# Optimization experiments

Measured on AMD Instinct MI355X. Metric: run time of the kernel, lower is better.

## Reference

```python
import jax, jax.numpy as jnp
import numpy as np

N = 50000
E = 1_600_000
IN_C = 128
HID = 64
HEADS = 2
OUT_C = 16
NEG_SLOPE = 0.2
EPS = 1e-16


def setup_inputs() -> dict:
    key = jax.random.key(0)
    ks = jax.random.split(key, 10)
    x = jax.random.normal(ks[0], (N, IN_C), dtype=jnp.float32)
    edge_index = jax.random.randint(ks[1], (2, E), 0, N, dtype=jnp.int64)
    # layer 1: in -> HEADS * HID, concat=True
    s1 = 1.0 / np.sqrt(IN_C)
    W1 = jax.random.normal(ks[2], (IN_C, HEADS * HID), dtype=jnp.float32) * s1
    att_src1 = jax.random.normal(ks[3], (HEADS, HID), dtype=jnp.float32) * (1.0 / np.sqrt(HID))
    att_dst1 = jax.random.normal(ks[4], (HEADS, HID), dtype=jnp.float32) * (1.0 / np.sqrt(HID))
    b1 = jnp.zeros((HEADS * HID,), dtype=jnp.float32)
    # layer 2: HEADS*HID -> OUT_C, heads=1
    s2 = 1.0 / np.sqrt(HEADS * HID)
    W2 = jax.random.normal(ks[5], (HEADS * HID, OUT_C), dtype=jnp.float32) * s2
    att_src2 = jax.random.normal(ks[6], (1, OUT_C), dtype=jnp.float32) * (1.0 / np.sqrt(OUT_C))
    att_dst2 = jax.random.normal(ks[7], (1, OUT_C), dtype=jnp.float32) * (1.0 / np.sqrt(OUT_C))
    b2 = jnp.zeros((OUT_C,), dtype=jnp.float32)
    return {"x": x, "W1": W1, "att_src1": att_src1, "att_dst1": att_dst1, "b1": b1,
            "W2": W2, "att_src2": att_src2, "att_dst2": att_dst2, "b2": b2,
            "edge_index": edge_index}


def gat_conv(x, edge_index, W, att_src, att_dst, bias, heads, out_ch):
    """PyG-style GATConv: per-head linear, additive attention, softmax over
    incoming edges of each destination node, scatter-add aggregation."""
    n = x.shape[0]
    src, dst = edge_index[0], edge_index[1]
    h = (x @ W).reshape(n, heads, out_ch)                # [N,H,C]
    a_src = jnp.einsum('nhc,hc->nh', h, att_src)          # [N,H]
    a_dst = jnp.einsum('nhc,hc->nh', h, att_dst)          # [N,H]
    e = a_src[src] + a_dst[dst]                           # [E,H]
    e = jnp.where(e >= 0, e, NEG_SLOPE * e)               # LeakyReLU(0.2)
    e_max = jax.ops.segment_max(e, dst, num_segments=n)   # [N,H]
    e_max = jax.lax.stop_gradient(jnp.where(jnp.isfinite(e_max), e_max, 0.0))
    e_exp = jnp.exp(e - e_max[dst])                       # [E,H]
    denom = jax.ops.segment_sum(e_exp, dst, num_segments=n)  # [N,H]
    alpha = e_exp / (denom[dst] + EPS)                    # [E,H]
    msg = h[src] * alpha[:, :, None]                      # [E,H,C] (dominant traffic)
    out = jax.ops.segment_sum(msg, dst, num_segments=n)   # [N,H,C]
    return out.reshape(n, heads * out_ch) + bias


def reference(x, W1, att_src1, att_dst1, b1, W2, att_src2, att_dst2, b2, edge_index):
    h = gat_conv(x, edge_index, W1, att_src1, att_dst1, b1, HEADS, HID)
    h = jax.nn.elu(h)
    h = gat_conv(h, edge_index, W2, att_src2, att_dst2, b2, 1, OUT_C)
    return jax.nn.softmax(h, axis=1)
```

## Files before the change

kernel.cpp:

```cpp
#include <hip/hip_runtime.h>
#include <hip/hip_fp16.h>
#include <cstdint>
#include <cstddef>

#define N_NODES 50000
#define N_EDGES 1600000
#define NEG_SLOPE 0.2f
#define GAT_EPS 1e-16f

#define NCHUNK 128
#define CE (N_EDGES / NCHUNK)
#define NBKT 196
#define GEMM_BLOCKS 782

typedef _Float16 half8v __attribute__((ext_vector_type(8)));
typedef float f32x4 __attribute__((ext_vector_type(4)));



__global__ __launch_bounds__(256) void k_prep_tiny(
    const float* __restrict__ W1, const float* __restrict__ W2,
    const float* __restrict__ b1,
    _Float16* __restrict__ w1t, float* __restrict__ w2tp, float* __restrict__ b1p) {
    int t = threadIdx.x, b = blockIdx.x;
    if (b < 8) {
        for (int i = t; i < 2048; i += 256) {
            int idx = b * 2048 + i;
            int c = idx >> 7, k = idx & 127;
            w1t[c * 136 + k] = (_Float16)W1[k * 128 + c];
        }
    } else {
        for (int i = t; i < 2112; i += 256) {
            int j = i / 132, kp = i % 132;
            if (kp < 128) {
                int real = (kp & 7) * 16 + (kp >> 3);
                w2tp[j * 132 + kp] = W2[real * 16 + j];
            } else {
                w2tp[j * 132 + kp] = 0.f;
            }
        }
        if (t < 128) {
            int real = (t & 7) * 16 + (t >> 3);
            b1p[t] = b1[real];
        }
    }
}


__global__ __launch_bounds__(256) void k_gh(
    const float* __restrict__ x, const _Float16* __restrict__ w1t,
    const float* __restrict__ att_src, const float* __restrict__ att_dst,
    _Float16* __restrict__ h1p, float* __restrict__ a_src, float* __restrict__ a_dst,
    const int* __restrict__ ei, int* __restrict__ coarse) {
    __shared__ __align__(16) char smem[34816];
    int t = threadIdx.x;
    int b = blockIdx.x;
    if (b >= GEMM_BLOCKS) {
        int* h = (int*)smem;
        int g = b - GEMM_BLOCKS;
        if (t < NBKT) h[t] = 0;
        __syncthreads();
        int e0 = g * CE;
        for (int e = e0 + t; e < e0 + CE; e += 256)
            atomicAdd(&h[ei[N_EDGES + e] >> 8], 1);
        __syncthreads();
        if (t < NBKT) coarse[t * NCHUNK + g] = h[t];
        return;
    }
    _Float16* wl = (_Float16*)smem;
    {
        const uint4* src = (const uint4*)w1t;
        uint4* dst = (uint4*)wl;
        for (int j = t; j < 2176; j += 256) dst[j] = src[j];
    }
    __syncthreads();
    int wv = t >> 6, lane = t & 63;
    int m = lane & 15, q = lane >> 4;
    int nb = b * 64 + wv * 16;
    int grow = nb + m;
    const float* xrow = x + (size_t)((grow < N_NODES) ? grow : (N_NODES - 1)) * 128;
    f32x4 acc[8];
#pragma unroll
    for (int ct = 0; ct < 8; ++ct) acc[ct] = (f32x4){0.f, 0.f, 0.f, 0.f};
#pragma unroll
    for (int kc = 0; kc < 4; ++kc) {
        float4 u0 = *(const float4*)(xrow + kc * 32 + q * 8);
        float4 u1 = *(const float4*)(xrow + kc * 32 + q * 8 + 4);
        half8v a;
        a[0] = (_Float16)u0.x; a[1] = (_Float16)u0.y;
        a[2] = (_Float16)u0.z; a[3] = (_Float16)u0.w;
        a[4] = (_Float16)u1.x; a[5] = (_Float16)u1.y;
        a[6] = (_Float16)u1.z; a[7] = (_Float16)u1.w;
#pragma unroll
        for (int ct = 0; ct < 8; ++ct) {
            half8v bf = *(const half8v*)(wl + (ct * 16 + m) * 136 + kc * 32 + q * 8);
            acc[ct] = __builtin_amdgcn_mfma_f32_16x16x32_f16(a, bf, acc[ct], 0, 0, 0);
        }
    }
    float att_s[8], att_d[8];
#pragma unroll
    for (int ct = 0; ct < 8; ++ct) {
        att_s[ct] = att_src[ct * 16 + m];
        att_d[ct] = att_dst[ct * 16 + m];
    }
#pragma unroll
    for (int r = 0; r < 4; ++r) {
        int gn = nb + q * 4 + r;
        half8v hv;
        float ps0 = 0.f, ps1 = 0.f, pd0 = 0.f, pd1 = 0.f;
#pragma unroll
        for (int ct = 0; ct < 8; ++ct) {
            float v = acc[ct][r];
            hv[ct] = (_Float16)v;
            if (ct < 4) { ps0 += v * att_s[ct]; pd0 += v * att_d[ct]; }
            else        { ps1 += v * att_s[ct]; pd1 += v * att_d[ct]; }
        }
#pragma unroll
        for (int off = 8; off >= 1; off >>= 1) {
            ps0 += __shfl_xor(ps0, off, 64);
            ps1 += __shfl_xor(ps1, off, 64);
            pd0 += __shfl_xor(pd0, off, 64);
            pd1 += __shfl_xor(pd1, off, 64);
        }
        if (gn < N_NODES) {
            *(half8v*)(h1p + (size_t)gn * 128 + m * 8) = hv;
            if (m == 0) {
                a_src[gn * 2 + 0] = ps0;
                a_src[gn * 2 + 1] = ps1;
                a_dst[gn * 2 + 0] = pd0;
                a_dst[gn * 2 + 1] = pd1;
            }
        }
    }
}


__global__ __launch_bounds__(1024) void k_cscan(const int* __restrict__ coarse,
                                                int* __restrict__ cbase,
                                                int* __restrict__ bb,
                                                int* __restrict__ row_start) {
    __shared__ int cl[NBKT * NCHUNK];
    __shared__ int btot[NBKT];
    __shared__ int bbase[NBKT];
    int t = threadIdx.x;
    for (int i = t; i < NBKT * NCHUNK; i += 1024) cl[i] = coarse[i];
    __syncthreads();
    if (t < NBKT) {
        int s = 0;
        for (int g = 0; g < NCHUNK; ++g) s += cl[t * NCHUNK + g];
        btot[t] = s;
    }
    __syncthreads();
    if (t == 0) {
        int base = 0;
        for (int b = 0; b < NBKT; ++b) { bbase[b] = base; base += btot[b]; }
    }
    __syncthreads();
    if (t < NBKT) {
        int run = bbase[t];
        bb[t] = run;
        for (int g = 0; g < NCHUNK; ++g) {
            cbase[t * NCHUNK + g] = run;
            run += cl[t * NCHUNK + g];
        }
    }
    if (t == 0) { bb[NBKT] = N_EDGES; row_start[N_NODES] = N_EDGES; }
}

__global__ __launch_bounds__(256) void k_partition(const int* __restrict__ ei,
                                                   const int* __restrict__ cbase,
                                                   int2* __restrict__ part) {
    __shared__ int loc[NBKT];
    int t = threadIdx.x, g = blockIdx.x;
    if (t < NBKT) loc[t] = cbase[t * NCHUNK + g];
    __syncthreads();
    int e0 = g * CE;
    for (int e = e0 + t; e < e0 + CE; e += 256) {
        int s = ei[e], d = ei[N_EDGES + e];
        int slot = atomicAdd(&loc[d >> 8], 1);
        part[slot] = make_int2(s, d);
    }
}

__global__ __launch_bounds__(256) void k_local(const int2* __restrict__ part,
                                               const int* __restrict__ bb,
                                               const float* __restrict__ a_src1,
                                               const float* __restrict__ a_dst1,
                                               int* __restrict__ row_start,
                                               int4* __restrict__ csr) {
    __shared__ int hist[256];
    __shared__ int fillv[256];
    __shared__ float2 adl[256];
    __shared__ int wtot[4];
    int t = threadIdx.x, b = blockIdx.x;
    int n0 = b << 8;
    int es = bb[b], ee = bb[b + 1];
    hist[t] = 0;
    if (n0 + t < N_NODES) adl[t] = ((const float2*)a_dst1)[n0 + t];
    __syncthreads();
    for (int e = es + t; e < ee; e += 256) atomicAdd(&hist[part[e].y - n0], 1);
    __syncthreads();
    int lane = t & 63, w = t >> 6;
    int v = hist[t], x = v;
#pragma unroll
    for (int off = 1; off < 64; off <<= 1) {
        int y = __shfl_up(x, off, 64);
        if (lane >= off) x += y;
    }
    if (lane == 63) wtot[w] = x;
    __syncthreads();
    int woff = 0;
    for (int i = 0; i < w; ++i) woff += wtot[i];
    int excl = woff + x - v;
    if (n0 + t < N_NODES) row_start[n0 + t] = es + excl;
    fillv[t] = excl;
    __syncthreads();
    for (int e = es + t; e < ee; e += 256) {
        int2 sd = part[e];
        int j = sd.y - n0;
        int slot = es + atomicAdd(&fillv[j], 1);
        float2 as = ((const float2*)a_src1)[sd.x];
        float2 ad = adl[j];
        float e0 = as.x + ad.x; e0 = (e0 >= 0.f) ? e0 : NEG_SLOPE * e0;
        float e1 = as.y + ad.y; e1 = (e1 >= 0.f) ? e1 : NEG_SLOPE * e1;
        csr[slot] = make_int4(sd.x, __float_as_int(expf(e0)), __float_as_int(expf(e1)), 0);
    }
}


__global__ __launch_bounds__(256) void k_agg1f(
    const int* __restrict__ row_start, const int4* __restrict__ csr,
    const _Float16* __restrict__ h1p, const float* __restrict__ b1p,
    const float* __restrict__ w2tp,
    const float* __restrict__ att_src2, const float* __restrict__ att_dst2,
    float* __restrict__ h2, float* __restrict__ as2, float* __restrict__ ad2) {
    __shared__ float w2l[16 * 132];
    __shared__ float rows[4][128];
    int t = threadIdx.x;
    for (int i = t; i < 528; i += 256) ((float4*)w2l)[i] = ((const float4*)w2tp)[i];
    __syncthreads();
    int wv = t >> 6, lane = t & 63;
    int d = blockIdx.x * 4 + wv;
    int row = row_start[d], end = row_start[d + 1];
    int half = lane >> 5;
    int L = lane & 31;
    int c0 = L * 4;
    int head = L & 1;
    float den = 0.f;
    float4 acc = make_float4(0.f, 0.f, 0.f, 0.f);
    int i = row;
    for (; i + 8 <= end; i += 8) {
#pragma unroll
        for (int p = 0; p < 4; ++p) {
            int idx = i + 2 * p + half;
            int4 e4 = csr[idx];
            int s = e4.x;
            float we = head ? __int_as_float(e4.z) : __int_as_float(e4.y);
            uint2 u = *(const uint2*)(h1p + (size_t)s * 128 + c0);
            __half2 p0 = *(__half2*)&u.x;
            __half2 p1 = *(__half2*)&u.y;
            float2 f0 = __half22float2(p0);
            float2 f1 = __half22float2(p1);
            den += we;
            acc.x += we * f0.x; acc.y += we * f0.y;
            acc.z += we * f1.x; acc.w += we * f1.y;
        }
    }
    for (; i < end; i += 2) {
        int idx = i + half;
        bool ok = idx < end;
        int idxc = ok ? idx : i;
        int4 e4 = csr[idxc];
        int s = e4.x;
        float we = head ? __int_as_float(e4.z) : __int_as_float(e4.y);
        if (!ok) we = 0.f;
        uint2 u = *(const uint2*)(h1p + (size_t)s * 128 + c0);
        __half2 p0 = *(__half2*)&u.x;
        __half2 p1 = *(__half2*)&u.y;
        float2 f0 = __half22float2(p0);
        float2 f1 = __half22float2(p1);
        den += we;
        acc.x += we * f0.x; acc.y += we * f0.y;
        acc.z += we * f1.x; acc.w += we * f1.y;
    }
    den += __shfl_xor(den, 32, 64);
    acc.x += __shfl_xor(acc.x, 32, 64);
    acc.y += __shfl_xor(acc.y, 32, 64);
    acc.z += __shfl_xor(acc.z, 32, 64);
    acc.w += __shfl_xor(acc.w, 32, 64);
    float inv = 1.f / (den + GAT_EPS);
    float4 bv = ((const float4*)b1p)[L];
    float o0 = acc.x * inv + bv.x;
    float o1 = acc.y * inv + bv.y;
    float o2 = acc.z * inv + bv.z;
    float o3 = acc.w * inv + bv.w;
    o0 = (o0 > 0.f) ? o0 : expm1f(o0);
    o1 = (o1 > 0.f) ? o1 : expm1f(o1);
    o2 = (o2 > 0.f) ? o2 : expm1f(o2);
    o3 = (o3 > 0.f) ? o3 : expm1f(o3);
    if (half == 0) *(float4*)(&rows[wv][c0]) = make_float4(o0, o1, o2, o3);
    int j = lane & 15, q = lane >> 4;
    const float* r = rows[wv];
    const float* wt = &w2l[j * 132];
    int k0 = q * 32;
    float acc2 = 0.f;
#pragma unroll
    for (int sI = 0; sI < 8; ++sI) {
        int sp = ((sI + q) & 7) * 4;
        float4 rv = *(const float4*)(r + k0 + sp);
        float4 w4 = *(const float4*)(wt + k0 + sp);
        acc2 += rv.x * w4.x + rv.y * w4.y + rv.z * w4.z + rv.w * w4.w;
    }
    acc2 += __shfl_xor(acc2, 16, 64);
    acc2 += __shfl_xor(acc2, 32, 64);
    if (lane < 16) {
        h2[(size_t)d * 16 + j] = acc2;
        float ps = acc2 * att_src2[j];
        float pd = acc2 * att_dst2[j];
#pragma unroll
        for (int off = 8; off >= 1; off >>= 1) {
            ps += __shfl_xor(ps, off, 64);
            pd += __shfl_xor(pd, off, 64);
        }
        if (lane == 0) { as2[d] = ps; ad2[d] = pd; }
    }
}


__global__ __launch_bounds__(256) void k_agg2(
    const int* __restrict__ row_start, const int4* __restrict__ csr,
    const float* __restrict__ h2, const float* __restrict__ as2,
    const float* __restrict__ ad2, const float* __restrict__ b2,
    float* __restrict__ out) {
    int t = threadIdx.x;
    int wv = t >> 6, lane = t & 63;
    int d = blockIdx.x * 4 + wv;
    int row = row_start[d], end = row_start[d + 1];
    float ad = ad2[d];
    int c = lane & 15, q = lane >> 4;
    float den = 0.f, acc = 0.f;
    for (int base = row; base < end; base += 64) {
        int idx = base + lane;
        float w = 0.f; int s = 0;
        if (idx < end) {
            s = csr[idx].x;
            float e = as2[s] + ad;
            e = (e >= 0.f) ? e : NEG_SLOPE * e;
            w = expf(e);
        }
        den += w;
        int m = end - base; if (m > 64) m = 64;
        int jj = 0;
        for (; jj + 8 <= m; jj += 8) {
            float w0 = __shfl(w, jj + q, 64);
            int   s0 = __shfl(s, jj + q, 64);
            float w1_ = __shfl(w, jj + 4 + q, 64);
            int   s1 = __shfl(s, jj + 4 + q, 64);
            float h0 = h2[(size_t)s0 * 16 + c];
            float h1_ = h2[(size_t)s1 * 16 + c];
            acc += w0 * h0 + w1_ * h1_;
        }
        for (; jj < m; jj += 4) {
            float wj = __shfl(w, jj + q, 64);
            int sj = __shfl(s, jj + q, 64);
            acc += wj * h2[(size_t)sj * 16 + c];
        }
    }
#pragma unroll
    for (int off = 32; off >= 1; off >>= 1) den += __shfl_xor(den, off, 64);
    acc += __shfl_xor(acc, 16, 64);
    acc += __shfl_xor(acc, 32, 64);
    float v = acc / (den + GAT_EPS) + b2[c];
    float mmax = v;
#pragma unroll
    for (int off = 8; off >= 1; off >>= 1) mmax = fmaxf(mmax, __shfl_xor(mmax, off, 16));
    float ex = expf(v - mmax);
    float sum = ex;
#pragma unroll
    for (int off = 8; off >= 1; off >>= 1) sum += __shfl_xor(sum, off, 16);
    if (lane < 16) out[(size_t)d * 16 + c] = ex / sum;
}


extern "C" void kernel_launch(void* const* d_in, const int* in_sizes, int n_in,
                              void* d_out, int out_size, void* d_ws, size_t ws_size,
                              hipStream_t stream) {
    const float* x        = (const float*)d_in[0];
    const float* W1       = (const float*)d_in[1];
    const float* att_src1 = (const float*)d_in[2];
    const float* att_dst1 = (const float*)d_in[3];
    const float* b1       = (const float*)d_in[4];
    const float* W2       = (const float*)d_in[5];
    const float* att_src2 = (const float*)d_in[6];
    const float* att_dst2 = (const float*)d_in[7];
    const float* b2       = (const float*)d_in[8];
    const int*   ei       = (const int*)d_in[9];

    char* p = (char*)d_ws;
    auto alloc = [&](size_t bytes) {
        char* r = p;
        p += (bytes + 255) & ~(size_t)255;
        return r;
    };
    _Float16* h1p  = (_Float16*)alloc(sizeof(_Float16) * (size_t)N_NODES * 128);
    _Float16* w1t  = (_Float16*)alloc(sizeof(_Float16) * 128 * 136);
    float* w2tp    = (float*)alloc(sizeof(float) * 16 * 132);
    float* b1p     = (float*)alloc(sizeof(float) * 128);
    float* h2      = (float*)alloc(sizeof(float) * (size_t)N_NODES * 16);
    float* a_src   = (float*)alloc(sizeof(float) * N_NODES * 2);
    float* a_dst   = (float*)alloc(sizeof(float) * N_NODES * 2);
    float* as2     = (float*)alloc(sizeof(float) * N_NODES);
    float* ad2     = (float*)alloc(sizeof(float) * N_NODES);
    int* coarse    = (int*)alloc(sizeof(int) * NBKT * NCHUNK);
    int* cbase     = (int*)alloc(sizeof(int) * NBKT * NCHUNK);
    int* bb        = (int*)alloc(sizeof(int) * (NBKT + 1));
    int* row_start = (int*)alloc(sizeof(int) * (N_NODES + 1));
    int2* part     = (int2*)alloc(sizeof(int2) * (size_t)N_EDGES);
    int4* csr      = (int4*)alloc(sizeof(int4) * (size_t)N_EDGES);

    k_prep_tiny<<<9, 256, 0, stream>>>(W1, W2, b1, w1t, w2tp, b1p);
    k_gh<<<GEMM_BLOCKS + NCHUNK, 256, 0, stream>>>(x, w1t, att_src1, att_dst1, h1p, a_src, a_dst, ei, coarse);
    k_cscan<<<1, 1024, 0, stream>>>(coarse, cbase, bb, row_start);
    k_partition<<<NCHUNK, 256, 0, stream>>>(ei, cbase, part);
    k_local<<<NBKT, 256, 0, stream>>>(part, bb, a_src, a_dst, row_start, csr);
    k_agg1f<<<N_NODES / 4, 256, 0, stream>>>(row_start, csr, h1p, b1p, w2tp, att_src2, att_dst2, h2, as2, ad2);
    k_agg2<<<N_NODES / 4, 256, 0, stream>>>(row_start, csr, h2, as2, ad2, b2, (float*)d_out);
}
```

Measured before the change: 267.2 us.

## Fold weight prep into GEMM kernel and use nontemporal CSR loads

Removes the separate prep kernel launch. Each GEMM block now transposes and converts W1 into shared memory directly from global fp32, and one extra block prepares the W2/b1 layouts. CSR edge reads in both aggregation kernels use nontemporal loads, so the streamed edge records do not evict the reused feature rows from cache. In exchange, every GEMM block repeats the W1 transpose with uncoalesced, bank-conflicting shared stores instead of a contiguous copy.

```diff
diff --git a/kernel.cpp b/kernel.cpp
--- a/kernel.cpp
+++ b/kernel.cpp
@@ -14,47 +14,38 @@
 #define GEMM_BLOCKS 782
 
 typedef _Float16 half8v __attribute__((ext_vector_type(8)));
+typedef _Float16 half4v __attribute__((ext_vector_type(4)));
 typedef float f32x4 __attribute__((ext_vector_type(4)));
-
-
-
-__global__ __launch_bounds__(256) void k_prep_tiny(
-    const float* __restrict__ W1, const float* __restrict__ W2,
-    const float* __restrict__ b1,
-    _Float16* __restrict__ w1t, float* __restrict__ w2tp, float* __restrict__ b1p) {
-    int t = threadIdx.x, b = blockIdx.x;
-    if (b < 8) {
-        for (int i = t; i < 2048; i += 256) {
-            int idx = b * 2048 + i;
-            int c = idx >> 7, k = idx & 127;
-            w1t[c * 136 + k] = (_Float16)W1[k * 128 + c];
-        }
-    } else {
+typedef int i32x4 __attribute__((ext_vector_type(4)));
+
+
+
+__global__ __launch_bounds__(256) void k_gh(
+    const float* __restrict__ x, const float* __restrict__ W1,
+    const float* __restrict__ W2, const float* __restrict__ b1,
+    const float* __restrict__ att_src, const float* __restrict__ att_dst,
+    _Float16* __restrict__ h1p, float* __restrict__ a_src, float* __restrict__ a_dst,
+    const int* __restrict__ ei, int* __restrict__ coarse,
+    float* __restrict__ w2tp, float* __restrict__ b1p) {
+    __shared__ __align__(16) char smem[34816];
+    int t = threadIdx.x;
+    int b = blockIdx.x;
+    if (b == GEMM_BLOCKS + NCHUNK) {
         for (int i = t; i < 2112; i += 256) {
             int j = i / 132, kp = i % 132;
+            float v = 0.f;
             if (kp < 128) {
                 int real = (kp & 7) * 16 + (kp >> 3);
-                w2tp[j * 132 + kp] = W2[real * 16 + j];
-            } else {
-                w2tp[j * 132 + kp] = 0.f;
+                v = W2[real * 16 + j];
             }
+            w2tp[i] = v;
         }
         if (t < 128) {
             int real = (t & 7) * 16 + (t >> 3);
             b1p[t] = b1[real];
         }
-    }
-}
-
-
-__global__ __launch_bounds__(256) void k_gh(
-    const float* __restrict__ x, const _Float16* __restrict__ w1t,
-    const float* __restrict__ att_src, const float* __restrict__ att_dst,
-    _Float16* __restrict__ h1p, float* __restrict__ a_src, float* __restrict__ a_dst,
-    const int* __restrict__ ei, int* __restrict__ coarse) {
-    __shared__ __align__(16) char smem[34816];
-    int t = threadIdx.x;
-    int b = blockIdx.x;
+        return;
+    }
     if (b >= GEMM_BLOCKS) {
         int* h = (int*)smem;
         int g = b - GEMM_BLOCKS;
@@ -68,10 +59,9 @@
         return;
     }
     _Float16* wl = (_Float16*)smem;
-    {
-        const uint4* src = (const uint4*)w1t;
-        uint4* dst = (uint4*)wl;
-        for (int j = t; j < 2176; j += 256) dst[j] = src[j];
+    for (int j = t; j < 16384; j += 256) {
+        int k = j >> 7, c = j & 127;
+        wl[c * 136 + k] = (_Float16)W1[j];
     }
     __syncthreads();
     int wv = t >> 6, lane = t & 63;
@@ -229,7 +219,7 @@
 
 
 __global__ __launch_bounds__(256) void k_agg1f(
-    const int* __restrict__ row_start, const int4* __restrict__ csr,
+    const int* __restrict__ row_start, const int* __restrict__ csr_i,
     const _Float16* __restrict__ h1p, const float* __restrict__ b1p,
     const float* __restrict__ w2tp,
     const float* __restrict__ att_src2, const float* __restrict__ att_dst2,
@@ -239,6 +229,7 @@
     int t = threadIdx.x;
     for (int i = t; i < 528; i += 256) ((float4*)w2l)[i] = ((const float4*)w2tp)[i];
     __syncthreads();
+    const i32x4* csr = (const i32x4*)csr_i;
     int wv = t >> 6, lane = t & 63;
     int d = blockIdx.x * 4 + wv;
     int row = row_start[d], end = row_start[d + 1];
@@ -253,35 +244,31 @@
 #pragma unroll
         for (int p = 0; p < 4; ++p) {
             int idx = i + 2 * p + half;
-            int4 e4 = csr[idx];
-            int s = e4.x;
-            float we = head ? __int_as_float(e4.z) : __int_as_float(e4.y);
-            uint2 u = *(const uint2*)(h1p + (size_t)s * 128 + c0);
-            __half2 p0 = *(__half2*)&u.x;
-            __half2 p1 = *(__half2*)&u.y;
-            float2 f0 = __half22float2(p0);
-            float2 f1 = __half22float2(p1);
+            i32x4 e4 = __builtin_nontemporal_load(&csr[idx]);
+            int s = e4[0];
+            float we = head ? __int_as_float(e4[2]) : __int_as_float(e4[1]);
+            half4v hv = *(const half4v*)(h1p + (size_t)s * 128 + c0);
             den += we;
-            acc.x += we * f0.x; acc.y += we * f0.y;
-            acc.z += we * f1.x; acc.w += we * f1.y;
+            acc.x += we * (float)hv[0];
+            acc.y += we * (float)hv[1];
+            acc.z += we * (float)hv[2];
+            acc.w += we * (float)hv[3];
         }
     }
     for (; i < end; i += 2) {
         int idx = i + half;
         bool ok = idx < end;
         int idxc = ok ? idx : i;
-        int4 e4 = csr[idxc];
-        int s = e4.x;
-        float we = head ? __int_as_float(e4.z) : __int_as_float(e4.y);
+        i32x4 e4 = __builtin_nontemporal_load(&csr[idxc]);
+        int s = e4[0];
+        float we = head ? __int_as_float(e4[2]) : __int_as_float(e4[1]);
         if (!ok) we = 0.f;
-        uint2 u = *(const uint2*)(h1p + (size_t)s * 128 + c0);
-        __half2 p0 = *(__half2*)&u.x;
-        __half2 p1 = *(__half2*)&u.y;
-        float2 f0 = __half22float2(p0);
-        float2 f1 = __half22float2(p1);
+        half4v hv = *(const half4v*)(h1p + (size_t)s * 128 + c0);
         den += we;
-        acc.x += we * f0.x; acc.y += we * f0.y;
-        acc.z += we * f1.x; acc.w += we * f1.y;
+        acc.x += we * (float)hv[0];
+        acc.y += we * (float)hv[1];
+        acc.z += we * (float)hv[2];
+        acc.w += we * (float)hv[3];
     }
     den += __shfl_xor(den, 32, 64);
     acc.x += __shfl_xor(acc.x, 32, 64);
@@ -328,7 +315,7 @@
 
 
 __global__ __launch_bounds__(256) void k_agg2(
-    const int* __restrict__ row_start, const int4* __restrict__ csr,
+    const int* __restrict__ row_start, const int* __restrict__ csr_i,
     const float* __restrict__ h2, const float* __restrict__ as2,
     const float* __restrict__ ad2, const float* __restrict__ b2,
     float* __restrict__ out) {
@@ -343,7 +330,7 @@
         int idx = base + lane;
         float w = 0.f; int s = 0;
         if (idx < end) {
-            s = csr[idx].x;
+            s = __builtin_nontemporal_load(csr_i + (size_t)idx * 4);
             float e = as2[s] + ad;
             e = (e >= 0.f) ? e : NEG_SLOPE * e;
             w = expf(e);
@@ -403,7 +390,6 @@
         return r;
     };
     _Float16* h1p  = (_Float16*)alloc(sizeof(_Float16) * (size_t)N_NODES * 128);
-    _Float16* w1t  = (_Float16*)alloc(sizeof(_Float16) * 128 * 136);
     float* w2tp    = (float*)alloc(sizeof(float) * 16 * 132);
     float* b1p     = (float*)alloc(sizeof(float) * 128);
     float* h2      = (float*)alloc(sizeof(float) * (size_t)N_NODES * 16);
@@ -418,11 +404,11 @@
     int2* part     = (int2*)alloc(sizeof(int2) * (size_t)N_EDGES);
     int4* csr      = (int4*)alloc(sizeof(int4) * (size_t)N_EDGES);
 
-    k_prep_tiny<<<9, 256, 0, stream>>>(W1, W2, b1, w1t, w2tp, b1p);
-    k_gh<<<GEMM_BLOCKS + NCHUNK, 256, 0, stream>>>(x, w1t, att_src1, att_dst1, h1p, a_src, a_dst, ei, coarse);
+    k_gh<<<GEMM_BLOCKS + NCHUNK + 1, 256, 0, stream>>>(x, W1, W2, b1, att_src1, att_dst1,
+                                                       h1p, a_src, a_dst, ei, coarse, w2tp, b1p);
     k_cscan<<<1, 1024, 0, stream>>>(coarse, cbase, bb, row_start);
     k_partition<<<NCHUNK, 256, 0, stream>>>(ei, cbase, part);
     k_local<<<NBKT, 256, 0, stream>>>(part, bb, a_src, a_dst, row_start, csr);
-    k_agg1f<<<N_NODES / 4, 256, 0, stream>>>(row_start, csr, h1p, b1p, w2tp, att_src2, att_dst2, h2, as2, ad2);
-    k_agg2<<<N_NODES / 4, 256, 0, stream>>>(row_start, csr, h2, as2, ad2, b2, (float*)d_out);
-}
+    k_agg1f<<<N_NODES / 4, 256, 0, stream>>>(row_start, (const int*)csr, h1p, b1p, w2tp, att_src2, att_dst2, h2, as2, ad2);
+    k_agg2<<<N_NODES / 4, 256, 0, stream>>>(row_start, (const int*)csr, h2, as2, ad2, b2, (float*)d_out);
+}
```

Result: slower. 278.9 us (+4.4%).
